# Performance work log

Hardware: AMD Instinct MI355X
Metric: run time of the kernel (lower is better)

## Reference

```python
import jax, jax.numpy as jnp
import numpy as np

N_NODES = 100000


def _gcn_conv(x, src, dst, w_edge, W, b, n_nodes):
    # PyG GCNConv: deg computed at target (col) with self-loop weights included
    deg = jax.ops.segment_sum(w_edge, dst, num_segments=n_nodes)
    dinv = jnp.where(deg > 0, jax.lax.rsqrt(deg), 0.0)
    norm = dinv[src] * w_edge * dinv[dst]            # [E+N]
    h = x @ W                                        # [N, out] linear (no bias yet)
    msg = norm[:, None] * h[src]                     # gather + scale, [E+N, out]
    out = jax.ops.segment_sum(msg, dst, num_segments=n_nodes)  # scatter-add at target
    return out + b


def setup_inputs() -> dict:
    key = jax.random.key(0)
    k1, k2, k3, k4, k5 = jax.random.split(key, 5)
    n, din, dh, dout = N_NODES, 128, 128, 64
    E = 1600000
    x = jax.random.normal(k1, (n, din), dtype=jnp.float32)
    edge_index = jax.random.randint(k2, (2, E), 0, n, dtype=jnp.int64)
    # Glorot-ish init for layer weights, zero bias (PyG default)
    W1 = jax.random.normal(k3, (din, dh), dtype=jnp.float32) / np.sqrt(din)
    b1 = jnp.zeros((dh,), dtype=jnp.float32)
    W2 = jax.random.normal(k4, (dh, dout), dtype=jnp.float32) / np.sqrt(dh)
    b2 = jnp.zeros((dout,), dtype=jnp.float32)
    return {"x": x, "edge_index": edge_index, "W1": W1, "b1": b1, "W2": W2, "b2": b2}


def reference(x, edge_index, W1, b1, W2, b2):
    n = x.shape[0]
    # add self-loops with weight 1 (PyG add_self_loops + fill_value=1)
    loop = jnp.arange(n, dtype=edge_index.dtype)
    src = jnp.concatenate([edge_index[0], loop])
    dst = jnp.concatenate([edge_index[1], loop])
    w_edge = jnp.ones(src.shape[0], dtype=x.dtype)

    h = _gcn_conv(x, src, dst, w_edge, W1, b1, n)
    h = jax.nn.relu(h)
    # dropout: eval mode (identity)
    out = _gcn_conv(h, src, dst, w_edge, W2, b2, n)
    return out
```

## Files before the change

### kernel.cpp

```cpp
#include <hip/hip_runtime.h>

typedef _Float16 half2v __attribute__((ext_vector_type(2)));
typedef _Float16 half4v __attribute__((ext_vector_type(4)));
typedef _Float16 f16x8 __attribute__((ext_vector_type(8)));
typedef float f32x4 __attribute__((ext_vector_type(4)));

#define NBKT_MAX 256
#define BKT_CAP  16384
#define OVF_CAP  8192
#define SRC_MASK 0x1FFFF

__global__ void wcast_kernel(const float* __restrict__ W, _Float16* __restrict__ Wt) {
    int t = blockIdx.x * 256 + threadIdx.x;
    if (t < 128 * 128) {
        int k = t >> 7, c = t & 127;
        Wt[c * 128 + k] = (_Float16)W[k * 128 + c];
    }
}

__global__ void scan1_kernel(const int* __restrict__ deg, int* __restrict__ rowstart,
                             int* __restrict__ blockSums, float* __restrict__ dinv, int n) {
    __shared__ int tmp[256];
    int t = threadIdx.x;
    int i = blockIdx.x * 256 + t;
    int v = (i < n) ? deg[i] : 0;
    if (i < n) dinv[i] = rsqrtf((float)(v + 1));
    tmp[t] = v;
    __syncthreads();
#pragma unroll
    for (int off = 1; off < 256; off <<= 1) {
        int add = (t >= off) ? tmp[t - off] : 0;
        __syncthreads();
        tmp[t] += add;
        __syncthreads();
    }
    if (i < n) rowstart[i] = tmp[t] - v;
    if (t == 255) blockSums[blockIdx.x] = tmp[255];
}

__global__ void scan2_kernel(int* __restrict__ blockSums, int nb) {
    __shared__ int tmp[512];
    int t = threadIdx.x;
    int v = (t < nb) ? blockSums[t] : 0;
    tmp[t] = v;
    __syncthreads();
#pragma unroll
    for (int off = 1; off < 512; off <<= 1) {
        int add = (t >= off) ? tmp[t - off] : 0;
        __syncthreads();
        tmp[t] += add;
        __syncthreads();
    }
    if (t < nb) blockSums[t] = tmp[t] - v;
}

__global__ __launch_bounds__(256) void scan3_scale_kernel(
        int* __restrict__ rowstart, const int* __restrict__ blockSums,
        _Float16* __restrict__ h1, const float* __restrict__ dinv, int n) {
    int j = blockIdx.x * 256 + threadIdx.x;
    if (j < n) rowstart[j] += blockSums[j >> 8];
    if (j < n * 16) {
        float dv = dinv[j >> 4];
        f16x8 v = ((const f16x8*)h1)[j];
#pragma unroll
        for (int k = 0; k < 8; k++) v[k] = (_Float16)((float)v[k] * dv);
        ((f16x8*)h1)[j] = v;
    }
}

__global__ __launch_bounds__(256) void part_gemm1_kernel(
        const int* __restrict__ src, const int* __restrict__ dst,
        int* __restrict__ bktCnt, int* __restrict__ ovfCnt,
        int2* __restrict__ ovfBuf, unsigned* __restrict__ pairPart, int E,
        const float* __restrict__ x, const _Float16* __restrict__ Wt,
        _Float16* __restrict__ h, int n, int nbkt) {
    __shared__ union {
        _Float16 xs_h[64][128];
        struct { int cnt[NBKT_MAX]; int gbase[NBKT_MAX]; int off[NBKT_MAX]; } s;
    } u;
    int bid = blockIdx.x;
    int t = threadIdx.x;
    if (bid % 5 != 4) {
        int gb = (bid / 5) * 4 + (bid % 5);
        int node0 = gb * 64;
        if (node0 >= n) return;

#pragma unroll
        for (int i = 0; i < 4; i++) {
            int fi = t + 256 * i;
            int row = fi >> 4, seg = fi & 15;
            float4 a = make_float4(0.f, 0.f, 0.f, 0.f);
            float4 b4 = make_float4(0.f, 0.f, 0.f, 0.f);
            if (node0 + row < n) {
                const float4* xr = (const float4*)(x + (size_t)(node0 + row) * 128 + seg * 8);
                a = xr[0]; b4 = xr[1];
            }
            f16x8 hv;
            hv[0] = (_Float16)a.x;  hv[1] = (_Float16)a.y;
            hv[2] = (_Float16)a.z;  hv[3] = (_Float16)a.w;
            hv[4] = (_Float16)b4.x; hv[5] = (_Float16)b4.y;
            hv[6] = (_Float16)b4.z; hv[7] = (_Float16)b4.w;
            int byte = row * 256 + ((seg * 16) ^ ((row & 7) << 4));
            *(f16x8*)((char*)&u.xs_h[0][0] + byte) = hv;
        }
        __syncthreads();

        int wid = t >> 6, l = t & 63;
        int row0 = wid * 16;
        int arow = row0 + (l & 15);
        int kgrp = l >> 4;
        f32x4 acc[8];
#pragma unroll
        for (int ct = 0; ct < 8; ct++) acc[ct] = (f32x4){0.f, 0.f, 0.f, 0.f};

        const char* xbase = (const char*)&u.xs_h[0][0] + arow * 256;
#pragma unroll
        for (int ks = 0; ks < 4; ks++) {
            int abyte = ((ks * 64 + kgrp * 16) ^ ((arow & 7) << 4));
            f16x8 afrag = *(const f16x8*)(xbase + abyte);
#pragma unroll
            for (int ct = 0; ct < 8; ct++) {
                f16x8 bfrag = *(const f16x8*)(Wt + (ct * 16 + (l & 15)) * 128 + ks * 32 + kgrp * 8);
                acc[ct] = __builtin_amdgcn_mfma_f32_16x16x32_f16(afrag, bfrag, acc[ct], 0, 0, 0);
            }
        }

        int r0 = row0 + kgrp * 4;
#pragma unroll
        for (int ct = 0; ct < 8; ct++) {
            int col = ct * 16 + (l & 15);
#pragma unroll
            for (int r = 0; r < 4; r++) {
                int node = node0 + r0 + r;
                if (node < n)
                    h[(size_t)node * 128 + col] = (_Float16)acc[ct][r];
            }
        }
    } else {
        int sb = bid / 5;
        int base = sb * 4096;
        if (base >= E) return;
        int eend = base + 4096; if (eend > E) eend = E;
        for (int i = t; i < nbkt; i += 256) u.s.cnt[i] = 0;
        __syncthreads();
        for (int e0 = base + t * 8; e0 < eend; e0 += 2048) {
            if (e0 + 8 <= eend) {
                int4 d0 = *(const int4*)(dst + e0);
                int4 d1 = *(const int4*)(dst + e0 + 4);
                atomicAdd(&u.s.cnt[d0.x >> 9], 1); atomicAdd(&u.s.cnt[d0.y >> 9], 1);
                atomicAdd(&u.s.cnt[d0.z >> 9], 1); atomicAdd(&u.s.cnt[d0.w >> 9], 1);
                atomicAdd(&u.s.cnt[d1.x >> 9], 1); atomicAdd(&u.s.cnt[d1.y >> 9], 1);
                atomicAdd(&u.s.cnt[d1.z >> 9], 1); atomicAdd(&u.s.cnt[d1.w >> 9], 1);
            } else {
                for (int e = e0; e < eend; e++) atomicAdd(&u.s.cnt[dst[e] >> 9], 1);
            }
        }
        __syncthreads();
        for (int i = t; i < nbkt; i += 256) {
            u.s.off[i] = 0;
            int c = u.s.cnt[i];
            if (c > 0) u.s.gbase[i] = atomicAdd(&bktCnt[i], c);
        }
        __syncthreads();
        for (int e0 = base + t * 8; e0 < eend; e0 += 2048) {
            if (e0 + 8 <= eend) {
                int4 s0 = *(const int4*)(src + e0);
                int4 s1 = *(const int4*)(src + e0 + 4);
                int4 d0 = *(const int4*)(dst + e0);
                int4 d1 = *(const int4*)(dst + e0 + 4);
                int ss[8] = {s0.x, s0.y, s0.z, s0.w, s1.x, s1.y, s1.z, s1.w};
                int dd[8] = {d0.x, d0.y, d0.z, d0.w, d1.x, d1.y, d1.z, d1.w};
#pragma unroll
                for (int j = 0; j < 8; j++) {
                    int b = dd[j] >> 9;
                    int slot = u.s.gbase[b] + atomicAdd(&u.s.off[b], 1);
                    unsigned p = ((unsigned)(dd[j] & 511) << 17) | (unsigned)ss[j];
                    if (slot < BKT_CAP) {
                        pairPart[(size_t)b * BKT_CAP + slot] = p;
                    } else {
                        int op = atomicAdd(ovfCnt, 1);
                        if (op < OVF_CAP) ovfBuf[op] = make_int2((int)p, b);
                    }
                }
            } else {
                for (int e = e0; e < eend; e++) {
                    int s = src[e], d = dst[e];
                    int b = d >> 9;
                    int slot = u.s.gbase[b] + atomicAdd(&u.s.off[b], 1);
                    unsigned p = ((unsigned)(d & 511) << 17) | (unsigned)s;
                    if (slot < BKT_CAP) {
                        pairPart[(size_t)b * BKT_CAP + slot] = p;
                    } else {
                        int op = atomicAdd(ovfCnt, 1);
                        if (op < OVF_CAP) ovfBuf[op] = make_int2((int)p, b);
                    }
                }
            }
        }
    }
}

__global__ __launch_bounds__(256) void deg_bucket_kernel(
        const unsigned* __restrict__ pairPart, const int* __restrict__ bktCnt,
        const int* __restrict__ ovfCnt, const int2* __restrict__ ovfBuf,
        int* __restrict__ deg, int n) {
    __shared__ int hist[512];
    int b = blockIdx.x;
    int t = threadIdx.x;
    hist[t] = 0; hist[t + 256] = 0;
    __syncthreads();
    int cnt = bktCnt[b];
    if (cnt > BKT_CAP) cnt = BKT_CAP;
    const unsigned* bp = pairPart + (size_t)b * BKT_CAP;
    for (int e0 = t * 4; e0 < cnt; e0 += 1024) {
        if (e0 + 4 <= cnt) {
            uint4 p = *(const uint4*)(bp + e0);
            atomicAdd(&hist[p.x >> 17], 1); atomicAdd(&hist[p.y >> 17], 1);
            atomicAdd(&hist[p.z >> 17], 1); atomicAdd(&hist[p.w >> 17], 1);
        } else {
            for (int e = e0; e < cnt; e++) atomicAdd(&hist[bp[e] >> 17], 1);
        }
    }
    int oc = *ovfCnt;
    if (oc > 0) {
        if (oc > OVF_CAP) oc = OVF_CAP;
        for (int i = t; i < oc; i += 256) {
            int2 p = ovfBuf[i];
            if (p.y == b) atomicAdd(&hist[((unsigned)p.x) >> 17], 1);
        }
    }
    __syncthreads();
    int node0 = b << 9;
    if (node0 + t < n)       deg[node0 + t]       = hist[t];
    if (node0 + t + 256 < n) deg[node0 + t + 256] = hist[t + 256];
}

__global__ __launch_bounds__(256) void scatter2_kernel(
        const unsigned* __restrict__ pairPart, const int* __restrict__ bktCnt,
        const int* __restrict__ ovfCnt, const int2* __restrict__ ovfBuf,
        const int* __restrict__ rowstart,
        int* __restrict__ srcSorted, int n) {
    __shared__ int lcur[512];
    int b = blockIdx.x;
    int t = threadIdx.x;
    int node0 = b << 9;
#pragma unroll
    for (int i = 0; i < 2; i++) {
        int node = node0 + t + 256 * i;
        if (node < n) lcur[t + 256 * i] = rowstart[node];
    }
    __syncthreads();
    int cnt = bktCnt[b];
    if (cnt > BKT_CAP) cnt = BKT_CAP;
    const unsigned* bp = pairPart + (size_t)b * BKT_CAP;
    for (int e0 = t * 4; e0 < cnt; e0 += 1024) {
        if (e0 + 4 <= cnt) {
            uint4 p = *(const uint4*)(bp + e0);
            int p0 = atomicAdd(&lcur[p.x >> 17], 1);
            int p1 = atomicAdd(&lcur[p.y >> 17], 1);
            int p2 = atomicAdd(&lcur[p.z >> 17], 1);
            int p3 = atomicAdd(&lcur[p.w >> 17], 1);
            srcSorted[p0] = (int)(p.x & SRC_MASK);
            srcSorted[p1] = (int)(p.y & SRC_MASK);
            srcSorted[p2] = (int)(p.z & SRC_MASK);
            srcSorted[p3] = (int)(p.w & SRC_MASK);
        } else {
            for (int e = e0; e < cnt; e++) {
                unsigned p = bp[e];
                int pos = atomicAdd(&lcur[p >> 17], 1);
                srcSorted[pos] = (int)(p & SRC_MASK);
            }
        }
    }
    int oc = *ovfCnt;
    if (oc > 0) {
        if (oc > OVF_CAP) oc = OVF_CAP;
        for (int i = t; i < oc; i += 256) {
            int2 p = ovfBuf[i];
            if (p.y == b) {
                int pos = atomicAdd(&lcur[((unsigned)p.x) >> 17], 1);
                srcSorted[pos] = (int)((unsigned)p.x & SRC_MASK);
            }
        }
    }
}

__global__ __launch_bounds__(256) void gather1_kernel(
        const int* __restrict__ srcS, const int* __restrict__ rowstart,
        const int* __restrict__ deg, const float* __restrict__ dinv,
        const _Float16* __restrict__ h1, const float* __restrict__ b1,
        float* __restrict__ h2, int n) {
    int t = threadIdx.x;
    int g = __builtin_amdgcn_readfirstlane(blockIdx.x * 4 + (t >> 6));
    int lane = t & 63;
    if (g >= n) return;

    float dg = dinv[g];
    half2v sv0 = ((const half2v*)(h1 + (size_t)g * 128))[lane];
    float2 acc = make_float2((float)sv0.x, (float)sv0.y);
    int beg = rowstart[g], end = beg + deg[g];
    int e = beg;
    while (e < end) {
        int rem = end - e;
        int sv = (lane < rem) ? srcS[e + lane] : 0;
        int chunk = rem < 64 ? rem : 64;
        int j = 0;
        for (; j + 8 <= chunk; j += 8) {
            int s0 = __shfl(sv, j + 0), s1 = __shfl(sv, j + 1);
            int s2 = __shfl(sv, j + 2), s3 = __shfl(sv, j + 3);
            int s4 = __shfl(sv, j + 4), s5 = __shfl(sv, j + 5);
            int s6 = __shfl(sv, j + 6), s7 = __shfl(sv, j + 7);
            half2v u0 = ((const half2v*)(h1 + (size_t)s0 * 128))[lane];
            half2v u1 = ((const half2v*)(h1 + (size_t)s1 * 128))[lane];
            half2v u2 = ((const half2v*)(h1 + (size_t)s2 * 128))[lane];
            half2v u3 = ((const half2v*)(h1 + (size_t)s3 * 128))[lane];
            half2v u4 = ((const half2v*)(h1 + (size_t)s4 * 128))[lane];
            half2v u5 = ((const half2v*)(h1 + (size_t)s5 * 128))[lane];
            half2v u6 = ((const half2v*)(h1 + (size_t)s6 * 128))[lane];
            half2v u7 = ((const half2v*)(h1 + (size_t)s7 * 128))[lane];
            acc.x += (float)u0.x; acc.y += (float)u0.y;
            acc.x += (float)u1.x; acc.y += (float)u1.y;
            acc.x += (float)u2.x; acc.y += (float)u2.y;
            acc.x += (float)u3.x; acc.y += (float)u3.y;
            acc.x += (float)u4.x; acc.y += (float)u4.y;
            acc.x += (float)u5.x; acc.y += (float)u5.y;
            acc.x += (float)u6.x; acc.y += (float)u6.y;
            acc.x += (float)u7.x; acc.y += (float)u7.y;
        }
        for (; j < chunk; j++) {
            int s = __shfl(sv, j);
            half2v u = ((const half2v*)(h1 + (size_t)s * 128))[lane];
            acc.x += (float)u.x; acc.y += (float)u.y;
        }
        e += chunk;
    }
    float2 b = ((const float2*)b1)[lane];
    acc.x = fmaxf(dg * acc.x + b.x, 0.f);
    acc.y = fmaxf(dg * acc.y + b.y, 0.f);
    ((float2*)(h2 + (size_t)g * 128))[lane] = acc;
}

__global__ __launch_bounds__(256) void gemm_nk64(const float* __restrict__ x,
                                                 const float* __restrict__ W,
                                                 const float* __restrict__ dinv,
                                                 _Float16* __restrict__ h, int n) {
    __shared__ float xs[32][128];
    int t = threadIdx.x;
    int node0 = blockIdx.x * 32;
#pragma unroll
    for (int i = 0; i < 4; i++) {
        int fi = t + 256 * i;
        int row = fi >> 5, cv = fi & 31;
        float4 v = make_float4(0.f, 0.f, 0.f, 0.f);
        if (node0 + row < n) v = ((const float4*)x)[(size_t)(node0 + row) * 32 + cv];
        ((float4*)(&xs[0][0]))[fi] = v;
    }
    __syncthreads();

    int tx = t & 15, ty = t >> 4;
    int c0 = tx * 4;
    float acc[2][4];
#pragma unroll
    for (int i = 0; i < 2; i++)
#pragma unroll
        for (int j = 0; j < 4; j++) acc[i][j] = 0.f;

    for (int k = 0; k < 128; k++) {
        float4 w = *(const float4*)(W + k * 64 + c0);
#pragma unroll
        for (int i = 0; i < 2; i++) {
            float xval = xs[ty + 16 * i][k];
            acc[i][0] += xval * w.x;
            acc[i][1] += xval * w.y;
            acc[i][2] += xval * w.z;
            acc[i][3] += xval * w.w;
        }
    }
#pragma unroll
    for (int i = 0; i < 2; i++) {
        int node = node0 + ty + 16 * i;
        if (node < n) {
            float dv = dinv[node];
            half4v hv;
            hv.x = (_Float16)(acc[i][0] * dv);
            hv.y = (_Float16)(acc[i][1] * dv);
            hv.z = (_Float16)(acc[i][2] * dv);
            hv.w = (_Float16)(acc[i][3] * dv);
            *(half4v*)(h + (size_t)node * 64 + c0) = hv;
        }
    }
}

__global__ __launch_bounds__(256) void gather2_kernel(
        const int* __restrict__ srcS, const int* __restrict__ rowstart,
        const int* __restrict__ deg, const float* __restrict__ dinv,
        const _Float16* __restrict__ h3, const float* __restrict__ b2,
        float* __restrict__ out, int n) {
    int t = threadIdx.x;
    int g = __builtin_amdgcn_readfirstlane(blockIdx.x * 4 + (t >> 6));
    int lane = t & 63;
    if (g >= n) return;
    float dg = dinv[g];
    float acc = (float)h3[(size_t)g * 64 + lane];
    int beg = rowstart[g], end = beg + deg[g];
    int e = beg;
    while (e < end) {
        int rem = end - e;
        int sv = (lane < rem) ? srcS[e + lane] : 0;
        int chunk = rem < 64 ? rem : 64;
        int j = 0;
        for (; j + 8 <= chunk; j += 8) {
            int s0 = __shfl(sv, j + 0), s1 = __shfl(sv, j + 1);
            int s2 = __shfl(sv, j + 2), s3 = __shfl(sv, j + 3);
            int s4 = __shfl(sv, j + 4), s5 = __shfl(sv, j + 5);
            int s6 = __shfl(sv, j + 6), s7 = __shfl(sv, j + 7);
            float u0 = (float)h3[(size_t)s0 * 64 + lane];
            float u1 = (float)h3[(size_t)s1 * 64 + lane];
            float u2 = (float)h3[(size_t)s2 * 64 + lane];
            float u3 = (float)h3[(size_t)s3 * 64 + lane];
            float u4 = (float)h3[(size_t)s4 * 64 + lane];
            float u5 = (float)h3[(size_t)s5 * 64 + lane];
            float u6 = (float)h3[(size_t)s6 * 64 + lane];
            float u7 = (float)h3[(size_t)s7 * 64 + lane];
            acc += u0 + u1 + u2 + u3 + u4 + u5 + u6 + u7;
        }
        for (; j < chunk; j++) {
            int s = __shfl(sv, j);
            acc += (float)h3[(size_t)s * 64 + lane];
        }
        e += chunk;
    }
    out[(size_t)g * 64 + lane] = dg * acc + b2[lane];
}

extern "C" void kernel_launch(void* const* d_in, const int* in_sizes, int n_in,
                              void* d_out, int out_size, void* d_ws, size_t ws_size,
                              hipStream_t stream) {
    const float* x  = (const float*)d_in[0];
    const int*   ei = (const int*)d_in[1];
    const float* W1 = (const float*)d_in[2];
    const float* b1 = (const float*)d_in[3];
    const float* W2 = (const float*)d_in[4];
    const float* b2 = (const float*)d_in[5];
    float* out = (float*)d_out;

    const int n = in_sizes[0] / 128;
    const int E = in_sizes[1] / 2;
    const int* src = ei;
    const int* dst = ei + E;
    const int nb = (n + 255) / 256;
    const int nbkt = (n + 511) >> 9;

    char* ws = (char*)d_ws;
    size_t off = 0;
    auto carve = [&](size_t bytes) -> char* {
        char* p = ws + off;
        off += (bytes + 255) & ~(size_t)255;
        return p;
    };
    int*   bktCnt    = (int*)carve((size_t)NBKT_MAX * 4);
    int*   ovfCnt    = (int*)carve(4);
    size_t msz       = (size_t)((char*)ovfCnt - (char*)bktCnt) + 256;
    int*   deg       = (int*)carve((size_t)n * 4);
    float* dinv      = (float*)carve((size_t)n * 4);
    int*   rowstart  = (int*)carve((size_t)n * 4);
    int*   blockSums = (int*)carve((size_t)nb * 4);
    int*   srcSorted = (int*)carve((size_t)E * 4);
    _Float16* Wt     = (_Float16*)carve((size_t)128 * 128 * 2);
    int2*  ovfBuf    = (int2*)carve((size_t)OVF_CAP * 8);
    _Float16* h1     = (_Float16*)carve((size_t)n * 128 * 2);
    float* bufB      = (float*)carve((size_t)n * 128 * 4);
    unsigned* pairPart = (unsigned*)bufB;
    _Float16* h3     = h1;

    hipMemsetAsync(bktCnt, 0, msz, stream);

    wcast_kernel<<<64, 256, 0, stream>>>(W1, Wt);

    int sortBlocks = (E + 4095) / 4096;
    int gemmBlocks = (n + 63) / 64;
    int gGroups = (gemmBlocks + 3) / 4;
    int groups = (sortBlocks > gGroups) ? sortBlocks : gGroups;
    int G = groups * 5;
    part_gemm1_kernel<<<G, 256, 0, stream>>>(src, dst, bktCnt, ovfCnt, ovfBuf,
                                             pairPart, E, x, Wt, h1, n, nbkt);

    deg_bucket_kernel<<<nbkt, 256, 0, stream>>>(pairPart, bktCnt, ovfCnt, ovfBuf, deg, n);

    scan1_kernel<<<nb, 256, 0, stream>>>(deg, rowstart, blockSums, dinv, n);
    scan2_kernel<<<1, 512, 0, stream>>>(blockSums, nb);
    scan3_scale_kernel<<<(n * 16 + 255) / 256, 256, 0, stream>>>(rowstart, blockSums, h1, dinv, n);

    scatter2_kernel<<<nbkt, 256, 0, stream>>>(pairPart, bktCnt, ovfCnt, ovfBuf,
                                              rowstart, srcSorted, n);

    gather1_kernel<<<(n + 3) / 4, 256, 0, stream>>>(srcSorted, rowstart, deg, dinv,
                                                    h1, b1, bufB, n);

    gemm_nk64<<<(n + 31) / 32, 256, 0, stream>>>(bufB, W2, dinv, h3, n);
    gather2_kernel<<<(n + 3) / 4, 256, 0, stream>>>(srcSorted, rowstart, deg, dinv,
                                                    h3, b2, out, n);
}
```

Measured before the change: 345.6 us.

## Fuse degree histogram with block scan; widen gather loads to split wave halves

Merges the per-bucket degree histogram and the first-level prefix scan into one 512-thread kernel, so deg, dinv, rowstart and block sums come out of a single pass and one launch plus a deg round trip disappear. Both gather kernels now split each wave into two halves that handle alternating neighbours with wider vector loads (half4 / half2 per lane), then combine the halves with a cross-half shuffle. This aims to raise memory-level parallelism on the random row gathers, at the cost of extra shuffles, idle half-lanes on odd tails, and a 512-thread scan block.

```diff
diff --git a/kernel.cpp b/kernel.cpp
--- a/kernel.cpp
+++ b/kernel.cpp
@@ -15,56 +15,6 @@
     if (t < 128 * 128) {
         int k = t >> 7, c = t & 127;
         Wt[c * 128 + k] = (_Float16)W[k * 128 + c];
-    }
-}
-
-__global__ void scan1_kernel(const int* __restrict__ deg, int* __restrict__ rowstart,
-                             int* __restrict__ blockSums, float* __restrict__ dinv, int n) {
-    __shared__ int tmp[256];
-    int t = threadIdx.x;
-    int i = blockIdx.x * 256 + t;
-    int v = (i < n) ? deg[i] : 0;
-    if (i < n) dinv[i] = rsqrtf((float)(v + 1));
-    tmp[t] = v;
-    __syncthreads();
-#pragma unroll
-    for (int off = 1; off < 256; off <<= 1) {
-        int add = (t >= off) ? tmp[t - off] : 0;
-        __syncthreads();
-        tmp[t] += add;
-        __syncthreads();
-    }
-    if (i < n) rowstart[i] = tmp[t] - v;
-    if (t == 255) blockSums[blockIdx.x] = tmp[255];
-}
-
-__global__ void scan2_kernel(int* __restrict__ blockSums, int nb) {
-    __shared__ int tmp[512];
-    int t = threadIdx.x;
-    int v = (t < nb) ? blockSums[t] : 0;
-    tmp[t] = v;
-    __syncthreads();
-#pragma unroll
-    for (int off = 1; off < 512; off <<= 1) {
-        int add = (t >= off) ? tmp[t - off] : 0;
-        __syncthreads();
-        tmp[t] += add;
-        __syncthreads();
-    }
-    if (t < nb) blockSums[t] = tmp[t] - v;
-}
-
-__global__ __launch_bounds__(256) void scan3_scale_kernel(
-        int* __restrict__ rowstart, const int* __restrict__ blockSums,
-        _Float16* __restrict__ h1, const float* __restrict__ dinv, int n) {
-    int j = blockIdx.x * 256 + threadIdx.x;
-    if (j < n) rowstart[j] += blockSums[j >> 8];
-    if (j < n * 16) {
-        float dv = dinv[j >> 4];
-        f16x8 v = ((const f16x8*)h1)[j];
-#pragma unroll
-        for (int k = 0; k < 8; k++) v[k] = (_Float16)((float)v[k] * dv);
-        ((f16x8*)h1)[j] = v;
     }
 }
 
@@ -200,19 +150,20 @@
     }
 }
 
-__global__ __launch_bounds__(256) void deg_bucket_kernel(
+__global__ __launch_bounds__(512) void deg_scan_kernel(
         const unsigned* __restrict__ pairPart, const int* __restrict__ bktCnt,
         const int* __restrict__ ovfCnt, const int2* __restrict__ ovfBuf,
-        int* __restrict__ deg, int n) {
+        int* __restrict__ deg, float* __restrict__ dinv, int* __restrict__ rowstart,
+        int* __restrict__ blockSums, int n) {
     __shared__ int hist[512];
     int b = blockIdx.x;
     int t = threadIdx.x;
-    hist[t] = 0; hist[t + 256] = 0;
+    hist[t] = 0;
     __syncthreads();
     int cnt = bktCnt[b];
     if (cnt > BKT_CAP) cnt = BKT_CAP;
     const unsigned* bp = pairPart + (size_t)b * BKT_CAP;
-    for (int e0 = t * 4; e0 < cnt; e0 += 1024) {
+    for (int e0 = t * 4; e0 < cnt; e0 += 2048) {
         if (e0 + 4 <= cnt) {
             uint4 p = *(const uint4*)(bp + e0);
             atomicAdd(&hist[p.x >> 17], 1); atomicAdd(&hist[p.y >> 17], 1);
@@ -224,15 +175,57 @@
     int oc = *ovfCnt;
     if (oc > 0) {
         if (oc > OVF_CAP) oc = OVF_CAP;
-        for (int i = t; i < oc; i += 256) {
+        for (int i = t; i < oc; i += 512) {
             int2 p = ovfBuf[i];
             if (p.y == b) atomicAdd(&hist[((unsigned)p.x) >> 17], 1);
         }
     }
     __syncthreads();
-    int node0 = b << 9;
-    if (node0 + t < n)       deg[node0 + t]       = hist[t];
-    if (node0 + t + 256 < n) deg[node0 + t + 256] = hist[t + 256];
+    int v = hist[t];
+#pragma unroll
+    for (int off = 1; off < 512; off <<= 1) {
+        int add = (t >= off) ? hist[t - off] : 0;
+        __syncthreads();
+        hist[t] += add;
+        __syncthreads();
+    }
+    int node = (b << 9) + t;
+    if (node < n) {
+        deg[node] = v;
+        dinv[node] = rsqrtf((float)(v + 1));
+        rowstart[node] = hist[t] - v;
+    }
+    if (t == 511) blockSums[b] = hist[511];
+}
+
+__global__ void scan2_kernel(int* __restrict__ blockSums, int nb) {
+    __shared__ int tmp[512];
+    int t = threadIdx.x;
+    int v = (t < nb) ? blockSums[t] : 0;
+    tmp[t] = v;
+    __syncthreads();
+#pragma unroll
+    for (int off = 1; off < 512; off <<= 1) {
+        int add = (t >= off) ? tmp[t - off] : 0;
+        __syncthreads();
+        tmp[t] += add;
+        __syncthreads();
+    }
+    if (t < nb) blockSums[t] = tmp[t] - v;
+}
+
+__global__ __launch_bounds__(256) void scan3_scale_kernel(
+        int* __restrict__ rowstart, const int* __restrict__ blockSums,
+        _Float16* __restrict__ h1, const float* __restrict__ dinv, int n) {
+    int j = blockIdx.x * 256 + threadIdx.x;
+    if (j < n) rowstart[j] += blockSums[j >> 9];
+    if (j < n * 16) {
+        float dv = dinv[j >> 4];
+        f16x8 v = ((const f16x8*)h1)[j];
+#pragma unroll
+        for (int k = 0; k < 8; k++) v[k] = (_Float16)((float)v[k] * dv);
+        ((f16x8*)h1)[j] = v;
+    }
 }
 
 __global__ __launch_bounds__(256) void scatter2_kernel(
@@ -294,10 +287,15 @@
     int g = __builtin_amdgcn_readfirstlane(blockIdx.x * 4 + (t >> 6));
     int lane = t & 63;
     if (g >= n) return;
-
+    int c = lane & 31;
+    int hsel = lane >> 5;
+
+    float4 acc = make_float4(0.f, 0.f, 0.f, 0.f);
+    if (hsel == 0) {
+        half4v v = ((const half4v*)(h1 + (size_t)g * 128))[c];
+        acc.x = (float)v.x; acc.y = (float)v.y; acc.z = (float)v.z; acc.w = (float)v.w;
+    }
     float dg = dinv[g];
-    half2v sv0 = ((const half2v*)(h1 + (size_t)g * 128))[lane];
-    float2 acc = make_float2((float)sv0.x, (float)sv0.y);
     int beg = rowstart[g], end = beg + deg[g];
     int e = beg;
     while (e < end) {
@@ -305,39 +303,54 @@
         int sv = (lane < rem) ? srcS[e + lane] : 0;
         int chunk = rem < 64 ? rem : 64;
         int j = 0;
-        for (; j + 8 <= chunk; j += 8) {
-            int s0 = __shfl(sv, j + 0), s1 = __shfl(sv, j + 1);
-            int s2 = __shfl(sv, j + 2), s3 = __shfl(sv, j + 3);
-            int s4 = __shfl(sv, j + 4), s5 = __shfl(sv, j + 5);
-            int s6 = __shfl(sv, j + 6), s7 = __shfl(sv, j + 7);
-            half2v u0 = ((const half2v*)(h1 + (size_t)s0 * 128))[lane];
-            half2v u1 = ((const half2v*)(h1 + (size_t)s1 * 128))[lane];
-            half2v u2 = ((const half2v*)(h1 + (size_t)s2 * 128))[lane];
-            half2v u3 = ((const half2v*)(h1 + (size_t)s3 * 128))[lane];
-            half2v u4 = ((const half2v*)(h1 + (size_t)s4 * 128))[lane];
-            half2v u5 = ((const half2v*)(h1 + (size_t)s5 * 128))[lane];
-            half2v u6 = ((const half2v*)(h1 + (size_t)s6 * 128))[lane];
-            half2v u7 = ((const half2v*)(h1 + (size_t)s7 * 128))[lane];
-            acc.x += (float)u0.x; acc.y += (float)u0.y;
-            acc.x += (float)u1.x; acc.y += (float)u1.y;
-            acc.x += (float)u2.x; acc.y += (float)u2.y;
-            acc.x += (float)u3.x; acc.y += (float)u3.y;
-            acc.x += (float)u4.x; acc.y += (float)u4.y;
-            acc.x += (float)u5.x; acc.y += (float)u5.y;
-            acc.x += (float)u6.x; acc.y += (float)u6.y;
-            acc.x += (float)u7.x; acc.y += (float)u7.y;
-        }
-        for (; j < chunk; j++) {
+        for (; j + 16 <= chunk; j += 16) {
+            int s0 = __shfl(sv, j + 0  + hsel), s1 = __shfl(sv, j + 2  + hsel);
+            int s2 = __shfl(sv, j + 4  + hsel), s3 = __shfl(sv, j + 6  + hsel);
+            int s4 = __shfl(sv, j + 8  + hsel), s5 = __shfl(sv, j + 10 + hsel);
+            int s6 = __shfl(sv, j + 12 + hsel), s7 = __shfl(sv, j + 14 + hsel);
+            half4v u0 = ((const half4v*)(h1 + (size_t)s0 * 128))[c];
+            half4v u1 = ((const half4v*)(h1 + (size_t)s1 * 128))[c];
+            half4v u2 = ((const half4v*)(h1 + (size_t)s2 * 128))[c];
+            half4v u3 = ((const half4v*)(h1 + (size_t)s3 * 128))[c];
+            half4v u4 = ((const half4v*)(h1 + (size_t)s4 * 128))[c];
+            half4v u5 = ((const half4v*)(h1 + (size_t)s5 * 128))[c];
+            half4v u6 = ((const half4v*)(h1 + (size_t)s6 * 128))[c];
+            half4v u7 = ((const half4v*)(h1 + (size_t)s7 * 128))[c];
+            acc.x += (float)u0.x; acc.y += (float)u0.y; acc.z += (float)u0.z; acc.w += (float)u0.w;
+            acc.x += (float)u1.x; acc.y += (float)u1.y; acc.z += (float)u1.z; acc.w += (float)u1.w;
+            acc.x += (float)u2.x; acc.y += (float)u2.y; acc.z += (float)u2.z; acc.w += (float)u2.w;
+            acc.x += (float)u3.x; acc.y += (float)u3.y; acc.z += (float)u3.z; acc.w += (float)u3.w;
+            acc.x += (float)u4.x; acc.y += (float)u4.y; acc.z += (float)u4.z; acc.w += (float)u4.w;
+            acc.x += (float)u5.x; acc.y += (float)u5.y; acc.z += (float)u5.z; acc.w += (float)u5.w;
+            acc.x += (float)u6.x; acc.y += (float)u6.y; acc.z += (float)u6.z; acc.w += (float)u6.w;
+            acc.x += (float)u7.x; acc.y += (float)u7.y; acc.z += (float)u7.z; acc.w += (float)u7.w;
+        }
+        for (; j + 2 <= chunk; j += 2) {
+            int s = __shfl(sv, j + hsel);
+            half4v u = ((const half4v*)(h1 + (size_t)s * 128))[c];
+            acc.x += (float)u.x; acc.y += (float)u.y; acc.z += (float)u.z; acc.w += (float)u.w;
+        }
+        if (j < chunk) {
             int s = __shfl(sv, j);
-            half2v u = ((const half2v*)(h1 + (size_t)s * 128))[lane];
-            acc.x += (float)u.x; acc.y += (float)u.y;
+            if (hsel == 0) {
+                half4v u = ((const half4v*)(h1 + (size_t)s * 128))[c];
+                acc.x += (float)u.x; acc.y += (float)u.y; acc.z += (float)u.z; acc.w += (float)u.w;
+            }
         }
         e += chunk;
     }
-    float2 b = ((const float2*)b1)[lane];
-    acc.x = fmaxf(dg * acc.x + b.x, 0.f);
-    acc.y = fmaxf(dg * acc.y + b.y, 0.f);
-    ((float2*)(h2 + (size_t)g * 128))[lane] = acc;
+    acc.x += __shfl_xor(acc.x, 32);
+    acc.y += __shfl_xor(acc.y, 32);
+    acc.z += __shfl_xor(acc.z, 32);
+    acc.w += __shfl_xor(acc.w, 32);
+    if (hsel == 0) {
+        float4 b = ((const float4*)b1)[c];
+        acc.x = fmaxf(dg * acc.x + b.x, 0.f);
+        acc.y = fmaxf(dg * acc.y + b.y, 0.f);
+        acc.z = fmaxf(dg * acc.z + b.z, 0.f);
+        acc.w = fmaxf(dg * acc.w + b.w, 0.f);
+        ((float4*)(h2 + (size_t)g * 128))[c] = acc;
+    }
 }
 
 __global__ __launch_bounds__(256) void gemm_nk64(const float* __restrict__ x,
@@ -400,8 +413,15 @@
     int g = __builtin_amdgcn_readfirstlane(blockIdx.x * 4 + (t >> 6));
     int lane = t & 63;
     if (g >= n) return;
+    int c = lane & 31;
+    int hsel = lane >> 5;
+
+    float2 acc = make_float2(0.f, 0.f);
+    if (hsel == 0) {
+        half2v v = ((const half2v*)(h3 + (size_t)g * 64))[c];
+        acc.x = (float)v.x; acc.y = (float)v.y;
+    }
     float dg = dinv[g];
-    float acc = (float)h3[(size_t)g * 64 + lane];
     int beg = rowstart[g], end = beg + deg[g];
     int e = beg;
     while (e < end) {
@@ -409,28 +429,49 @@
         int sv = (lane < rem) ? srcS[e + lane] : 0;
         int chunk = rem < 64 ? rem : 64;
         int j = 0;
-        for (; j + 8 <= chunk; j += 8) {
-            int s0 = __shfl(sv, j + 0), s1 = __shfl(sv, j + 1);
-            int s2 = __shfl(sv, j + 2), s3 = __shfl(sv, j + 3);
-            int s4 = __shfl(sv, j + 4), s5 = __shfl(sv, j + 5);
-            int s6 = __shfl(sv, j + 6), s7 = __shfl(sv, j + 7);
-            float u0 = (float)h3[(size_t)s0 * 64 + lane];
-            float u1 = (float)h3[(size_t)s1 * 64 + lane];
-            float u2 = (float)h3[(size_t)s2 * 64 + lane];
-            float u3 = (float)h3[(size_t)s3 * 64 + lane];
-            float u4 = (float)h3[(size_t)s4 * 64 + lane];
-            float u5 = (float)h3[(size_t)s5 * 64 + lane];
-            float u6 = (float)h3[(size_t)s6 * 64 + lane];
-            float u7 = (float)h3[(size_t)s7 * 64 + lane];
-            acc += u0 + u1 + u2 + u3 + u4 + u5 + u6 + u7;
-        }
-        for (; j < chunk; j++) {
+        for (; j + 16 <= chunk; j += 16) {
+            int s0 = __shfl(sv, j + 0  + hsel), s1 = __shfl(sv, j + 2  + hsel);
+            int s2 = __shfl(sv, j + 4  + hsel), s3 = __shfl(sv, j + 6  + hsel);
+            int s4 = __shfl(sv, j + 8  + hsel), s5 = __shfl(sv, j + 10 + hsel);
+            int s6 = __shfl(sv, j + 12 + hsel), s7 = __shfl(sv, j + 14 + hsel);
+            half2v u0 = ((const half2v*)(h3 + (size_t)s0 * 64))[c];
+            half2v u1 = ((const half2v*)(h3 + (size_t)s1 * 64))[c];
+            half2v u2 = ((const half2v*)(h3 + (size_t)s2 * 64))[c];
+            half2v u3 = ((const half2v*)(h3 + (size_t)s3 * 64))[c];
+            half2v u4 = ((const half2v*)(h3 + (size_t)s4 * 64))[c];
+            half2v u5 = ((const half2v*)(h3 + (size_t)s5 * 64))[c];
+            half2v u6 = ((const half2v*)(h3 + (size_t)s6 * 64))[c];
+            half2v u7 = ((const half2v*)(h3 + (size_t)s7 * 64))[c];
+            acc.x += (float)u0.x; acc.y += (float)u0.y;
+            acc.x += (float)u1.x; acc.y += (float)u1.y;
+            acc.x += (float)u2.x; acc.y += (float)u2.y;
+            acc.x += (float)u3.x; acc.y += (float)u3.y;
+            acc.x += (float)u4.x; acc.y += (float)u4.y;
+            acc.x += (float)u5.x; acc.y += (float)u5.y;
+            acc.x += (float)u6.x; acc.y += (float)u6.y;
+            acc.x += (float)u7.x; acc.y += (float)u7.y;
+        }
+        for (; j + 2 <= chunk; j += 2) {
+            int s = __shfl(sv, j + hsel);
+            half2v u = ((const half2v*)(h3 + (size_t)s * 64))[c];
+            acc.x += (float)u.x; acc.y += (float)u.y;
+        }
+        if (j < chunk) {
             int s = __shfl(sv, j);
-            acc += (float)h3[(size_t)s * 64 + lane];
+            if (hsel == 0) {
+                half2v u = ((const half2v*)(h3 + (size_t)s * 64))[c];
+                acc.x += (float)u.x; acc.y += (float)u.y;
+            }
         }
         e += chunk;
     }
-    out[(size_t)g * 64 + lane] = dg * acc + b2[lane];
+    acc.x += __shfl_xor(acc.x, 32);
+    acc.y += __shfl_xor(acc.y, 32);
+    if (hsel == 0) {
+        float2 b = ((const float2*)b2)[c];
+        ((float2*)(out + (size_t)g * 64))[c] =
+            make_float2(dg * acc.x + b.x, dg * acc.y + b.y);
+    }
 }
 
 extern "C" void kernel_launch(void* const* d_in, const int* in_sizes, int n_in,
@@ -448,7 +489,6 @@
     const int E = in_sizes[1] / 2;
     const int* src = ei;
     const int* dst = ei + E;
-    const int nb = (n + 255) / 256;
     const int nbkt = (n + 511) >> 9;
 
     char* ws = (char*)d_ws;
@@ -464,7 +504,7 @@
     int*   deg       = (int*)carve((size_t)n * 4);
     float* dinv      = (float*)carve((size_t)n * 4);
     int*   rowstart  = (int*)carve((size_t)n * 4);
-    int*   blockSums = (int*)carve((size_t)nb * 4);
+    int*   blockSums = (int*)carve((size_t)NBKT_MAX * 4);
     int*   srcSorted = (int*)carve((size_t)E * 4);
     _Float16* Wt     = (_Float16*)carve((size_t)128 * 128 * 2);
     int2*  ovfBuf    = (int2*)carve((size_t)OVF_CAP * 8);
@@ -485,10 +525,9 @@
     part_gemm1_kernel<<<G, 256, 0, stream>>>(src, dst, bktCnt, ovfCnt, ovfBuf,
                                              pairPart, E, x, Wt, h1, n, nbkt);
 
-    deg_bucket_kernel<<<nbkt, 256, 0, stream>>>(pairPart, bktCnt, ovfCnt, ovfBuf, deg, n);
-
-    scan1_kernel<<<nb, 256, 0, stream>>>(deg, rowstart, blockSums, dinv, n);
-    scan2_kernel<<<1, 512, 0, stream>>>(blockSums, nb);
+    deg_scan_kernel<<<nbkt, 512, 0, stream>>>(pairPart, bktCnt, ovfCnt, ovfBuf,
+                                              deg, dinv, rowstart, blockSums, n);
+    scan2_kernel<<<1, 512, 0, stream>>>(blockSums, nbkt);
     scan3_scale_kernel<<<(n * 16 + 255) / 256, 256, 0, stream>>>(rowstart, blockSums, h1, dinv, n);
 
     scatter2_kernel<<<nbkt, 256, 0, stream>>>(pairPart, bktCnt, ovfCnt, ovfBuf,
```

New measurement: 345.0 us. About the same (-0.2%).

## Fuse degree histogram, prefix scans, CSR scatter and row scaling into one kernel

Applied to the files above, without the earlier changes.

Replaces the separate degree-histogram, three-stage scan, h1 row-scaling and scatter kernels with a single per-bucket kernel of 512 threads. Each block builds a global base by scanning the bucket counts itself, scans its local histogram, writes deg, dinv and rowstart, scatters sorted sources, then scales its own h1 rows by dinv. This is meant to remove four kernel launches and the global round trips of deg and blockSums. In exchange the h1 scaling runs on only about 200 blocks, and every block repeats the small bucket-count scan.

```diff
diff --git a/kernel.cpp b/kernel.cpp
--- a/kernel.cpp
+++ b/kernel.cpp
@@ -15,56 +15,6 @@
     if (t < 128 * 128) {
         int k = t >> 7, c = t & 127;
         Wt[c * 128 + k] = (_Float16)W[k * 128 + c];
-    }
-}
-
-__global__ void scan1_kernel(const int* __restrict__ deg, int* __restrict__ rowstart,
-                             int* __restrict__ blockSums, float* __restrict__ dinv, int n) {
-    __shared__ int tmp[256];
-    int t = threadIdx.x;
-    int i = blockIdx.x * 256 + t;
-    int v = (i < n) ? deg[i] : 0;
-    if (i < n) dinv[i] = rsqrtf((float)(v + 1));
-    tmp[t] = v;
-    __syncthreads();
-#pragma unroll
-    for (int off = 1; off < 256; off <<= 1) {
-        int add = (t >= off) ? tmp[t - off] : 0;
-        __syncthreads();
-        tmp[t] += add;
-        __syncthreads();
-    }
-    if (i < n) rowstart[i] = tmp[t] - v;
-    if (t == 255) blockSums[blockIdx.x] = tmp[255];
-}
-
-__global__ void scan2_kernel(int* __restrict__ blockSums, int nb) {
-    __shared__ int tmp[512];
-    int t = threadIdx.x;
-    int v = (t < nb) ? blockSums[t] : 0;
-    tmp[t] = v;
-    __syncthreads();
-#pragma unroll
-    for (int off = 1; off < 512; off <<= 1) {
-        int add = (t >= off) ? tmp[t - off] : 0;
-        __syncthreads();
-        tmp[t] += add;
-        __syncthreads();
-    }
-    if (t < nb) blockSums[t] = tmp[t] - v;
-}
-
-__global__ __launch_bounds__(256) void scan3_scale_kernel(
-        int* __restrict__ rowstart, const int* __restrict__ blockSums,
-        _Float16* __restrict__ h1, const float* __restrict__ dinv, int n) {
-    int j = blockIdx.x * 256 + threadIdx.x;
-    if (j < n) rowstart[j] += blockSums[j >> 8];
-    if (j < n * 16) {
-        float dv = dinv[j >> 4];
-        f16x8 v = ((const f16x8*)h1)[j];
-#pragma unroll
-        for (int k = 0; k < 8; k++) v[k] = (_Float16)((float)v[k] * dv);
-        ((f16x8*)h1)[j] = v;
     }
 }
 
@@ -200,19 +150,33 @@
     }
 }
 
-__global__ __launch_bounds__(256) void deg_bucket_kernel(
+__global__ __launch_bounds__(512) void bucket_process_kernel(
         const unsigned* __restrict__ pairPart, const int* __restrict__ bktCnt,
         const int* __restrict__ ovfCnt, const int2* __restrict__ ovfBuf,
-        int* __restrict__ deg, int n) {
+        int* __restrict__ deg, float* __restrict__ dinv, int* __restrict__ rowstart,
+        int* __restrict__ srcSorted, _Float16* __restrict__ h1, int n, int nbkt) {
     __shared__ int hist[512];
+    __shared__ float sdinv[512];
     int b = blockIdx.x;
     int t = threadIdx.x;
-    hist[t] = 0; hist[t + 256] = 0;
+
+    if (t < 256) hist[t] = (t < nbkt) ? bktCnt[t] : 0;
+    __syncthreads();
+    for (int off = 1; off < 256; off <<= 1) {
+        int add = (t < 256 && t >= off) ? hist[t - off] : 0;
+        __syncthreads();
+        if (t < 256) hist[t] += add;
+        __syncthreads();
+    }
+    int myBase = hist[b] - bktCnt[b];
+    __syncthreads();
+
+    hist[t] = 0;
     __syncthreads();
     int cnt = bktCnt[b];
     if (cnt > BKT_CAP) cnt = BKT_CAP;
     const unsigned* bp = pairPart + (size_t)b * BKT_CAP;
-    for (int e0 = t * 4; e0 < cnt; e0 += 1024) {
+    for (int e0 = t * 4; e0 < cnt; e0 += 2048) {
         if (e0 + 4 <= cnt) {
             uint4 p = *(const uint4*)(bp + e0);
             atomicAdd(&hist[p.x >> 17], 1); atomicAdd(&hist[p.y >> 17], 1);
@@ -224,42 +188,40 @@
     int oc = *ovfCnt;
     if (oc > 0) {
         if (oc > OVF_CAP) oc = OVF_CAP;
-        for (int i = t; i < oc; i += 256) {
+        for (int i = t; i < oc; i += 512) {
             int2 p = ovfBuf[i];
             if (p.y == b) atomicAdd(&hist[((unsigned)p.x) >> 17], 1);
         }
     }
     __syncthreads();
-    int node0 = b << 9;
-    if (node0 + t < n)       deg[node0 + t]       = hist[t];
-    if (node0 + t + 256 < n) deg[node0 + t + 256] = hist[t + 256];
-}
-
-__global__ __launch_bounds__(256) void scatter2_kernel(
-        const unsigned* __restrict__ pairPart, const int* __restrict__ bktCnt,
-        const int* __restrict__ ovfCnt, const int2* __restrict__ ovfBuf,
-        const int* __restrict__ rowstart,
-        int* __restrict__ srcSorted, int n) {
-    __shared__ int lcur[512];
-    int b = blockIdx.x;
-    int t = threadIdx.x;
-    int node0 = b << 9;
-#pragma unroll
-    for (int i = 0; i < 2; i++) {
-        int node = node0 + t + 256 * i;
-        if (node < n) lcur[t + 256 * i] = rowstart[node];
-    }
-    __syncthreads();
-    int cnt = bktCnt[b];
-    if (cnt > BKT_CAP) cnt = BKT_CAP;
-    const unsigned* bp = pairPart + (size_t)b * BKT_CAP;
-    for (int e0 = t * 4; e0 < cnt; e0 += 1024) {
+
+    int v = hist[t];
+#pragma unroll
+    for (int off = 1; off < 512; off <<= 1) {
+        int add = (t >= off) ? hist[t - off] : 0;
+        __syncthreads();
+        hist[t] += add;
+        __syncthreads();
+    }
+    int cur = myBase + hist[t] - v;
+    float dv = rsqrtf((float)(v + 1));
+    int node = (b << 9) + t;
+    if (node < n) {
+        deg[node] = v;
+        dinv[node] = dv;
+        rowstart[node] = cur;
+    }
+    sdinv[t] = dv;
+    hist[t] = cur;
+    __syncthreads();
+
+    for (int e0 = t * 4; e0 < cnt; e0 += 2048) {
         if (e0 + 4 <= cnt) {
             uint4 p = *(const uint4*)(bp + e0);
-            int p0 = atomicAdd(&lcur[p.x >> 17], 1);
-            int p1 = atomicAdd(&lcur[p.y >> 17], 1);
-            int p2 = atomicAdd(&lcur[p.z >> 17], 1);
-            int p3 = atomicAdd(&lcur[p.w >> 17], 1);
+            int p0 = atomicAdd(&hist[p.x >> 17], 1);
+            int p1 = atomicAdd(&hist[p.y >> 17], 1);
+            int p2 = atomicAdd(&hist[p.z >> 17], 1);
+            int p3 = atomicAdd(&hist[p.w >> 17], 1);
             srcSorted[p0] = (int)(p.x & SRC_MASK);
             srcSorted[p1] = (int)(p.y & SRC_MASK);
             srcSorted[p2] = (int)(p.z & SRC_MASK);
@@ -267,20 +229,32 @@
         } else {
             for (int e = e0; e < cnt; e++) {
                 unsigned p = bp[e];
-                int pos = atomicAdd(&lcur[p >> 17], 1);
+                int pos = atomicAdd(&hist[p >> 17], 1);
                 srcSorted[pos] = (int)(p & SRC_MASK);
             }
         }
     }
-    int oc = *ovfCnt;
     if (oc > 0) {
-        if (oc > OVF_CAP) oc = OVF_CAP;
-        for (int i = t; i < oc; i += 256) {
+        for (int i = t; i < oc; i += 512) {
             int2 p = ovfBuf[i];
             if (p.y == b) {
-                int pos = atomicAdd(&lcur[((unsigned)p.x) >> 17], 1);
+                int pos = atomicAdd(&hist[((unsigned)p.x) >> 17], 1);
                 srcSorted[pos] = (int)((unsigned)p.x & SRC_MASK);
             }
+        }
+    }
+
+    int node0 = b << 9;
+    int rows = n - node0; if (rows > 512) rows = 512;
+    if (rows > 0) {
+        int total = rows * 16;
+        f16x8* hrow = (f16x8*)(h1 + (size_t)node0 * 128);
+        for (int i = t; i < total; i += 512) {
+            float dvv = sdinv[i >> 4];
+            f16x8 vv = hrow[i];
+#pragma unroll
+            for (int k = 0; k < 8; k++) vv[k] = (_Float16)((float)vv[k] * dvv);
+            hrow[i] = vv;
         }
     }
 }
@@ -448,7 +422,6 @@
     const int E = in_sizes[1] / 2;
     const int* src = ei;
     const int* dst = ei + E;
-    const int nb = (n + 255) / 256;
     const int nbkt = (n + 511) >> 9;
 
     char* ws = (char*)d_ws;
@@ -464,7 +437,6 @@
     int*   deg       = (int*)carve((size_t)n * 4);
     float* dinv      = (float*)carve((size_t)n * 4);
     int*   rowstart  = (int*)carve((size_t)n * 4);
-    int*   blockSums = (int*)carve((size_t)nb * 4);
     int*   srcSorted = (int*)carve((size_t)E * 4);
     _Float16* Wt     = (_Float16*)carve((size_t)128 * 128 * 2);
     int2*  ovfBuf    = (int2*)carve((size_t)OVF_CAP * 8);
@@ -485,14 +457,9 @@
     part_gemm1_kernel<<<G, 256, 0, stream>>>(src, dst, bktCnt, ovfCnt, ovfBuf,
                                              pairPart, E, x, Wt, h1, n, nbkt);
 
-    deg_bucket_kernel<<<nbkt, 256, 0, stream>>>(pairPart, bktCnt, ovfCnt, ovfBuf, deg, n);
-
-    scan1_kernel<<<nb, 256, 0, stream>>>(deg, rowstart, blockSums, dinv, n);
-    scan2_kernel<<<1, 512, 0, stream>>>(blockSums, nb);
-    scan3_scale_kernel<<<(n * 16 + 255) / 256, 256, 0, stream>>>(rowstart, blockSums, h1, dinv, n);
-
-    scatter2_kernel<<<nbkt, 256, 0, stream>>>(pairPart, bktCnt, ovfCnt, ovfBuf,
-                                              rowstart, srcSorted, n);
+    bucket_process_kernel<<<nbkt, 512, 0, stream>>>(pairPart, bktCnt, ovfCnt, ovfBuf,
+                                                    deg, dinv, rowstart, srcSorted,
+                                                    h1, n, nbkt);
 
     gather1_kernel<<<(n + 3) / 4, 256, 0, stream>>>(srcSorted, rowstart, deg, dinv,
                                                     h1, b1, bufB, n);
```

Measured after the change: 335.1 us. 1.03x faster.
